# Kernel tuning notes

Hardware: AMD Instinct MI355X
Metric: run time of the kernel (lower is better)

Reference implementation:

```python
import jax, jax.numpy as jnp
import numpy as np

C = 128; L = 2; LMAX = 3; NB = 8
R_MAX = 5.0; P_CUT = 5.0; AVG_NEI = 16.0
DELTA_K = 0.2; K_CUT = 0.6; NKRBF = 128; DP = 8
B_GRAPHS = 8; N_ATOMS = 3200; N_EDGES = 51200; NEL = 10
SKIP = (2.0 + 1.0) ** -0.5  # skip_connection_factor with use_ewald=True
_LOFLM_NP = np.repeat(np.arange(4), [1, 3, 5, 7])  # l index of each of 16 lm slots
LOFLM = jnp.asarray(_LOFLM_NP)
LM1H = jnp.asarray(np.eye(4, dtype=np.float32)[_LOFLM_NP])  # [16,4] one-hot lm->l


def _k_grid_np():
    r = np.arange(-3, 4)
    g = np.stack(np.meshgrid(r, r, r, indexing='ij'), -1).reshape(-1, 3).astype(np.float32) * DELTA_K
    return g[np.linalg.norm(g, axis=1) <= K_CUT + 1e-6]  # [K,3], K=123


def _k_rbf_np(kg):
    d = np.linalg.norm(kg, axis=1)
    c = np.linspace(0.0, K_CUT, NKRBF).astype(np.float32)
    w = c[1] - c[0]
    return np.exp(-0.5 * ((d[:, None] - c[None, :]) / w) ** 2).astype(np.float32)


def _sph_harm(u):
    # real spherical harmonics, e3nn 'component' normalization, l=0..3 -> 16 comps
    x, y, z = u[:, 0], u[:, 1], u[:, 2]
    s3, s5, s15 = 3.0 ** 0.5, 5.0 ** 0.5, 15.0 ** 0.5
    c70, c105, c42, c7 = 70.0 ** 0.5 / 4.0, 105.0 ** 0.5, 42.0 ** 0.5 / 4.0, 7.0 ** 0.5 / 2.0
    comps = [jnp.ones_like(x),
             s3 * x, s3 * y, s3 * z,
             s15 * x * y, s15 * y * z, 0.5 * s5 * (3 * z * z - 1.0), s15 * x * z, 0.5 * s15 * (x * x - y * y),
             c70 * y * (3 * x * x - y * y), c105 * x * y * z, c42 * y * (5 * z * z - 1.0),
             c7 * z * (5 * z * z - 3.0), c42 * x * (5 * z * z - 1.0), 0.5 * c105 * z * (x * x - y * y),
             c70 * x * (x * x - 3 * y * y)]
    return jnp.stack(comps, axis=-1)


def _radial(r):
    # Bessel basis * polynomial cutoff envelope (p=5)
    n = jnp.arange(1, NB + 1, dtype=r.dtype)
    rb = jnp.sqrt(2.0 / R_MAX) * jnp.sin(n * jnp.pi * r[:, None] / R_MAX) / jnp.maximum(r, 1e-9)[:, None]
    uu = jnp.clip(r / R_MAX, 0.0, 1.0)
    p = P_CUT
    env = 1.0 - (p + 1.0) * (p + 2.0) / 2.0 * uu ** 5 + p * (p + 2.0) * uu ** 6 - p * (p + 1.0) / 2.0 * uu ** 7
    env = env * (r < R_MAX)
    return rb * env[:, None]


def _forward(positions, node_attrs, shifts, edge_index, batch, kgrid, krbf, W_embed, atomic_E, rW1, rb1, rW2, rb2, rW3, rb3, rW4, Wup, w2, w3, Wmix, Wr0, Wr1a, Wr1b, Wdown, WupE, Wpre1, bpre1, Wpre2, bpre2, Wm1, bm1, Wm2, bm2):
    silu = jax.nn.silu
    src, dst = edge_index[0], edge_index[1]
    vec = positions[dst] - positions[src] + shifts            # [E,3]
    r = jnp.linalg.norm(vec, axis=1)
    uvec = vec / jnp.maximum(r, 1e-9)[:, None]
    Y = _sph_harm(uvec)                                       # [E,16]
    ef = _radial(r)                                           # [E,8]
    h = node_attrs @ W_embed                                  # [N,C]
    e0 = jax.ops.segment_sum(node_attrs @ atomic_E, batch, num_segments=B_GRAPHS)
    # Ewald precompute (shared across layers, as in the torch code: dot/sinc computed once)
    dot = positions @ kgrid.T                                 # [N,K]
    sd = jnp.prod(jnp.sinc(0.5 * DELTA_K * positions), axis=1, keepdims=True)  # [N,1]
    cosd = sd * jnp.cos(dot)
    sind = sd * jnp.sin(dot)
    kdown = krbf @ Wdown                                      # [K,DP]
    energy = e0
    for i in range(L):
        # ---- Ewald block ----
        hres = h + silu(h @ Wpre1[i] + bpre1[i]) @ Wpre2[i] + bpre2[i]
        kfilter = kdown @ WupE[i]                             # [K,C]
        sfr = jax.ops.segment_sum(hres[:, None, :] * cosd[:, :, None], batch, num_segments=B_GRAPHS)  # [B,K,C]
        sfi = jax.ops.segment_sum(hres[:, None, :] * sind[:, :, None], batch, num_segments=B_GRAPHS)
        he = 0.01 * (jnp.einsum('nk,nkc->nc', cosd, (sfr * kfilter)[batch])
                     + jnp.einsum('nk,nkc->nc', sind, (sfi * kfilter)[batch]))
        he = silu(he @ Wm1[i] + bm1[i])
        he = silu(he @ Wm2[i] + bm2[i])
        # ---- equivariant interaction (channelwise TP with SH, radial-MLP weights) ----
        hu = h @ Wup[i]
        w = silu(ef @ rW1[i] + rb1[i])
        w = silu(w @ rW2[i] + rb2[i])
        w = silu(w @ rW3[i] + rb3[i])
        w = (w @ rW4[i]).reshape(-1, C, LMAX + 1)             # [E,C,4] per-(channel,l) weights
        we = jnp.take(w, LOFLM, axis=2)                       # [E,C,16]
        msg = we * hu[src][:, :, None] * Y[:, None, :]        # [E,C,16]
        A = jax.ops.segment_sum(msg, dst, num_segments=positions.shape[0]) / AVG_NEI  # [N,C,16]
        # ---- product basis (invariant contractions up to correlation 3) + residual sc ----
        scal = A[:, :, 0]
        inv2 = jnp.einsum('ncs,sl->ncl', A * A, LM1H)         # [N,C,4] per-l norms
        feats = scal + jnp.einsum('ncl,lc->nc', inv2, w2[i]) + scal * jnp.einsum('ncl,lc->nc', inv2, w3[i])
        hprod = feats @ Wmix[i] + h
        h = SKIP * (hprod + he)
        # ---- readout ----
        if i < L - 1:
            node_e = (h @ Wr0)[:, 0]
        else:
            node_e = (silu(h @ Wr1a) @ Wr1b)[:, 0]
        energy = energy + jax.ops.segment_sum(node_e, batch, num_segments=B_GRAPHS)
    return energy  # [B]


def setup_inputs() -> dict:
    ks = jax.random.split(jax.random.key(0), 32)
    def rn(i, shape, scale):
        return jax.random.normal(ks[i], shape, jnp.float32) * scale
    d = {}
    d['positions'] = jax.random.normal(ks[0], (N_ATOMS, 3), jnp.float32)
    d['node_attrs'] = jax.random.uniform(ks[1], (N_ATOMS, NEL), dtype=jnp.float32)
    d['shifts'] = jnp.zeros((N_EDGES, 3), jnp.float32)
    d['edge_index'] = jax.random.randint(ks[2], (2, N_EDGES), 0, N_ATOMS)
    d['batch'] = jnp.sort(jax.random.randint(ks[3], (N_ATOMS,), 0, B_GRAPHS))
    kg = _k_grid_np()
    d['kgrid'] = jnp.asarray(kg)
    d['krbf'] = jnp.asarray(_k_rbf_np(kg))
    d['W_embed'] = rn(4, (NEL, C), NEL ** -0.5)
    d['atomic_E'] = rn(5, (NEL,), 1.0)
    d['rW1'] = rn(6, (L, NB, 64), NB ** -0.5)
    d['rb1'] = jnp.zeros((L, 64), jnp.float32)
    d['rW2'] = rn(7, (L, 64, 64), 64 ** -0.5)
    d['rb2'] = jnp.zeros((L, 64), jnp.float32)
    d['rW3'] = rn(8, (L, 64, 64), 64 ** -0.5)
    d['rb3'] = jnp.zeros((L, 64), jnp.float32)
    d['rW4'] = rn(9, (L, 64, C * (LMAX + 1)), 64 ** -0.5)
    d['Wup'] = rn(10, (L, C, C), C ** -0.5)
    d['w2'] = rn(11, (L, LMAX + 1, C), 0.1)
    d['w3'] = rn(12, (L, LMAX + 1, C), 0.1)
    d['Wmix'] = rn(13, (L, C, C), C ** -0.5)
    d['Wr0'] = rn(14, (C, 1), C ** -0.5)
    d['Wr1a'] = rn(15, (C, 16), C ** -0.5)
    d['Wr1b'] = rn(16, (16, 1), 16 ** -0.5)
    d['Wdown'] = rn(17, (NKRBF, DP), NKRBF ** -0.5)
    d['WupE'] = rn(18, (L, DP, C), DP ** -0.5)
    d['Wpre1'] = rn(19, (L, C, C), C ** -0.5)
    d['bpre1'] = jnp.zeros((L, C), jnp.float32)
    d['Wpre2'] = rn(20, (L, C, C), C ** -0.5)
    d['bpre2'] = jnp.zeros((L, C), jnp.float32)
    d['Wm1'] = rn(21, (L, C, C), C ** -0.5)
    d['bm1'] = jnp.zeros((L, C), jnp.float32)
    d['Wm2'] = rn(22, (L, C, C), C ** -0.5)
    d['bm2'] = jnp.zeros((L, C), jnp.float32)
    return d


def reference(positions, node_attrs, shifts, edge_index, batch, kgrid, krbf, W_embed, atomic_E, rW1, rb1, rW2, rb2, rW3, rb3, rW4, Wup, w2, w3, Wmix, Wr0, Wr1a, Wr1b, Wdown, WupE, Wpre1, bpre1, Wpre2, bpre2, Wm1, bm1, Wm2, bm2):
    return _forward(positions, node_attrs, shifts, edge_index, batch, kgrid, krbf, W_embed, atomic_E, rW1, rb1, rW2, rb2, rW3, rb3, rW4, Wup, w2, w3, Wmix, Wr0, Wr1a, Wr1b, Wdown, WupE, Wpre1, bpre1, Wpre2, bpre2, Wm1, bm1, Wm2, bm2)
```

## Files before the change

kernel.cpp:

```cpp
#include <hip/hip_runtime.h>
#include <hip/hip_bf16.h>
#include <math.h>

constexpr int NA  = 3200;
constexpr int NE  = 51200;
constexpr int C   = 128;
constexpr int NK  = 123;
constexpr int NKP = 128;
constexpr int BG  = 8;
constexpr int SFSPLIT = 8;
constexpr float SKIPF = 0.57735026918962576f;
constexpr float AVGN  = 16.0f;
constexpr size_t SFSZ = (size_t)BG * NK * C;

__device__ __forceinline__ float dsilu(float x) { return x / (1.0f + expf(-x)); }

__device__ __forceinline__ unsigned short f2bf(float f) {
    unsigned int u = __float_as_uint(f);
    unsigned int r = (u + 0x7fffu + ((u >> 16) & 1u)) >> 16;
    return (unsigned short)r;
}
__device__ __forceinline__ float bf2f(unsigned short s) {
    return __uint_as_float(((unsigned int)s) << 16);
}

typedef __attribute__((ext_vector_type(8))) short short8;
typedef __attribute__((ext_vector_type(4))) float f32x4;

template <int K, int ACT, int OBF16, int LB = 0>
__global__ __launch_bounds__(256, 4) void gemm_kernel(
    const float* __restrict__ X, const float* __restrict__ W,
    const float* __restrict__ bias, void* __restrict__ outv,
    int M, int N)
{
    if (LB) {
        int L = blockIdx.z;
        W += (size_t)L * K * N;
        if (bias) bias += (size_t)L * N;
        outv = OBF16 ? (void*)((unsigned short*)outv + (size_t)L * M * N)
                     : (void*)((float*)outv + (size_t)L * M * N);
    }
    constexpr int K4 = K / 4;
    constexpr int BK  = (K < 64) ? K : 64;
    constexpr int BK4 = BK / 4;
    constexpr int BK4P = BK4 + 1;
    __shared__ float As[64 * BK4P * 4];
    __shared__ float Bs[BK * 64];
    const int tid = threadIdx.x;
    const int m0 = blockIdx.x * 64;
    const int n0 = blockIdx.y * 64;

    const float4* X4 = (const float4*)X;
    const float4* W4 = (const float4*)W;
    float4* As4 = (float4*)As;
    float4* Bs4 = (float4*)Bs;
    const int N4 = N >> 2;

    const int tx = tid & 15;
    const int ty = tid >> 4;
    float acc[4][4];
#pragma unroll
    for (int i = 0; i < 4; i++)
#pragma unroll
        for (int j = 0; j < 4; j++) acc[i][j] = 0.0f;

    for (int k0 = 0; k0 < K4; k0 += BK4) {
        if (k0) __syncthreads();
        for (int idx = tid; idx < 64 * BK4; idx += 256) {
            int r = idx / BK4, k4 = idx - r * BK4;
            As4[r * BK4P + k4] = X4[(size_t)(m0 + r) * K4 + k0 + k4];
        }
        for (int idx = tid; idx < BK * 16; idx += 256) {
            int kr = idx >> 4, c4 = idx & 15;
            Bs4[idx] = W4[(size_t)(k0 * 4 + kr) * N4 + (n0 >> 2) + c4];
        }
        __syncthreads();

#pragma unroll 4
        for (int k4 = 0; k4 < BK4; k4++) {
            float a[4][4];
#pragma unroll
            for (int i = 0; i < 4; i++) {
                float4 av = As4[(ty * 4 + i) * BK4P + k4];
                a[i][0] = av.x; a[i][1] = av.y; a[i][2] = av.z; a[i][3] = av.w;
            }
#pragma unroll
            for (int kk = 0; kk < 4; kk++) {
                float4 bv = Bs4[(k4 * 4 + kk) * 16 + tx];
#pragma unroll
                for (int i = 0; i < 4; i++) {
                    acc[i][0] += a[i][kk] * bv.x;
                    acc[i][1] += a[i][kk] * bv.y;
                    acc[i][2] += a[i][kk] * bv.z;
                    acc[i][3] += a[i][kk] * bv.w;
                }
            }
        }
    }

    float4 bv = make_float4(0.f, 0.f, 0.f, 0.f);
    if (bias) bv = ((const float4*)bias)[(n0 >> 2) + tx];
#pragma unroll
    for (int i = 0; i < 4; i++) {
        int row = m0 + ty * 4 + i;
        size_t o = (size_t)row * N + n0 + tx * 4;
        float4 v;
        v.x = acc[i][0] + bv.x; v.y = acc[i][1] + bv.y;
        v.z = acc[i][2] + bv.z; v.w = acc[i][3] + bv.w;
        if (ACT) { v.x = dsilu(v.x); v.y = dsilu(v.y); v.z = dsilu(v.z); v.w = dsilu(v.w); }
        if (OBF16) {
            ushort4 pk;
            pk.x = f2bf(v.x); pk.y = f2bf(v.y); pk.z = f2bf(v.z); pk.w = f2bf(v.w);
            *(ushort4*)((unsigned short*)outv + o) = pk;
        } else {
            *(float4*)((float*)outv + o) = v;
        }
    }
}

__global__ __launch_bounds__(256, 2) void k_pre(
    const float* __restrict__ h,
    const unsigned short* __restrict__ W1t, const float* __restrict__ b1,
    const unsigned short* __restrict__ Wut,
    const unsigned short* __restrict__ W2t, const float* __restrict__ b2,
    float* __restrict__ hu, float* __restrict__ hres)
{
    constexpr int MT = 32, ASH = 136;
    __shared__ unsigned short Xs[MT * ASH];
    __shared__ unsigned short Ts[MT * ASH];
    __shared__ unsigned short Ws[128 * ASH];
    const int tid = threadIdx.x;
    const int m0 = blockIdx.x * MT;

    for (int idx = tid; idx < MT * 32; idx += 256) {
        int r = idx >> 5, c4 = idx & 31;
        float4 v = ((const float4*)h)[(size_t)(m0 + r) * 32 + c4];
        ushort4 pk;
        pk.x = f2bf(v.x); pk.y = f2bf(v.y); pk.z = f2bf(v.z); pk.w = f2bf(v.w);
        *(ushort4*)(Xs + r * ASH + c4 * 4) = pk;
    }
    for (int idx = tid; idx < 128 * 16; idx += 256) {
        int r = idx >> 4, s = idx & 15;
        *(short8*)(Ws + r * ASH + s * 8) = ((const short8*)W1t)[(size_t)r * 16 + s];
    }
    __syncthreads();

    const int wave = tid >> 6;
    const int lane = tid & 63;
    const int q = lane >> 4;
    const int l16 = lane & 15;
    const int mh = (wave & 1) * 16;
    const int nh = (wave >> 1) * 64;

    f32x4 acc[4];
#pragma unroll
    for (int ni = 0; ni < 4; ni++) acc[ni] = (f32x4){0.f, 0.f, 0.f, 0.f};
#pragma unroll
    for (int kc = 0; kc < 4; kc++) {
        short8 a = *(const short8*)(Xs + (mh + l16) * ASH + kc * 32 + q * 8);
#pragma unroll
        for (int ni = 0; ni < 4; ni++) {
            short8 b = *(const short8*)(Ws + (nh + ni * 16 + l16) * ASH + kc * 32 + q * 8);
            acc[ni] = __builtin_amdgcn_mfma_f32_16x16x32_bf16(a, b, acc[ni], 0, 0, 0);
        }
    }
#pragma unroll
    for (int ni = 0; ni < 4; ni++) {
        float bv = b1[nh + ni * 16 + l16];
#pragma unroll
        for (int r = 0; r < 4; r++)
            Ts[(mh + q * 4 + r) * ASH + nh + ni * 16 + l16] = f2bf(dsilu(acc[ni][r] + bv));
    }
    __syncthreads();
    for (int idx = tid; idx < 128 * 16; idx += 256) {
        int r = idx >> 4, s = idx & 15;
        *(short8*)(Ws + r * ASH + s * 8) = ((const short8*)Wut)[(size_t)r * 16 + s];
    }
    __syncthreads();
#pragma unroll
    for (int ni = 0; ni < 4; ni++) acc[ni] = (f32x4){0.f, 0.f, 0.f, 0.f};
#pragma unroll
    for (int kc = 0; kc < 4; kc++) {
        short8 a = *(const short8*)(Xs + (mh + l16) * ASH + kc * 32 + q * 8);
#pragma unroll
        for (int ni = 0; ni < 4; ni++) {
            short8 b = *(const short8*)(Ws + (nh + ni * 16 + l16) * ASH + kc * 32 + q * 8);
            acc[ni] = __builtin_amdgcn_mfma_f32_16x16x32_bf16(a, b, acc[ni], 0, 0, 0);
        }
    }
#pragma unroll
    for (int ni = 0; ni < 4; ni++) {
#pragma unroll
        for (int r = 0; r < 4; r++)
            hu[(size_t)(m0 + mh + q * 4 + r) * C + nh + ni * 16 + l16] = acc[ni][r];
    }
    __syncthreads();
    for (int idx = tid; idx < 128 * 16; idx += 256) {
        int r = idx >> 4, s = idx & 15;
        *(short8*)(Ws + r * ASH + s * 8) = ((const short8*)W2t)[(size_t)r * 16 + s];
    }
    __syncthreads();
#pragma unroll
    for (int ni = 0; ni < 4; ni++) acc[ni] = (f32x4){0.f, 0.f, 0.f, 0.f};
#pragma unroll
    for (int kc = 0; kc < 4; kc++) {
        short8 a = *(const short8*)(Ts + (mh + l16) * ASH + kc * 32 + q * 8);
#pragma unroll
        for (int ni = 0; ni < 4; ni++) {
            short8 b = *(const short8*)(Ws + (nh + ni * 16 + l16) * ASH + kc * 32 + q * 8);
            acc[ni] = __builtin_amdgcn_mfma_f32_16x16x32_bf16(a, b, acc[ni], 0, 0, 0);
        }
    }
#pragma unroll
    for (int ni = 0; ni < 4; ni++) {
        float bv = b2[nh + ni * 16 + l16];
#pragma unroll
        for (int r = 0; r < 4; r++) {
            int row = m0 + mh + q * 4 + r;
            int col = nh + ni * 16 + l16;
            hres[(size_t)row * C + col] = acc[ni][r] + bv + h[(size_t)row * C + col];
        }
    }
}

__global__ __launch_bounds__(128, 2) void k_mlp_mfma(
    const unsigned short* __restrict__ X, const unsigned short* __restrict__ Wbase,
    const float* __restrict__ bbase, unsigned short* __restrict__ out)
{
    constexpr int MT = 128, AS = 72;
    __shared__ unsigned short Als[MT * AS];
    __shared__ unsigned short Bls[64 * AS];
    const int tid = threadIdx.x;
    const int m0 = blockIdx.x * MT;
    const int layer = (m0 >= NE) ? 1 : 0;
    const unsigned short* Wt = Wbase + (size_t)layer * 64 * 64;
    const float* bias = bbase + (size_t)layer * 64;

    for (int idx = tid; idx < MT * 8; idx += 128) {
        int r = idx >> 3, s = idx & 7;
        *(short8*)(Als + r * AS + s * 8) = ((const short8*)X)[(size_t)(m0 + r) * 8 + s];
    }
    for (int idx = tid; idx < 64 * 8; idx += 128) {
        int r = idx >> 3, s = idx & 7;
        *(short8*)(Bls + r * AS + s * 8) = ((const short8*)Wt)[(size_t)r * 8 + s];
    }
    __syncthreads();

    const int wave = tid >> 6;
    const int lane = tid & 63;
    const int q = lane >> 4;
    const int l16 = lane & 15;
    const int mw = wave * 64;

    f32x4 acc[4][4];
#pragma unroll
    for (int mi = 0; mi < 4; mi++)
#pragma unroll
        for (int ni = 0; ni < 4; ni++) acc[mi][ni] = (f32x4){0.f, 0.f, 0.f, 0.f};

#pragma unroll
    for (int kc = 0; kc < 2; kc++) {
        short8 a[4], b[4];
#pragma unroll
        for (int mi = 0; mi < 4; mi++)
            a[mi] = *(const short8*)(Als + (mw + mi * 16 + l16) * AS + kc * 32 + q * 8);
#pragma unroll
        for (int ni = 0; ni < 4; ni++)
            b[ni] = *(const short8*)(Bls + (ni * 16 + l16) * AS + kc * 32 + q * 8);
#pragma unroll
        for (int mi = 0; mi < 4; mi++)
#pragma unroll
            for (int ni = 0; ni < 4; ni++)
                acc[mi][ni] = __builtin_amdgcn_mfma_f32_16x16x32_bf16(a[mi], b[ni], acc[mi][ni], 0, 0, 0);
    }

#pragma unroll
    for (int ni = 0; ni < 4; ni++) {
        float bv = bias[ni * 16 + l16];
#pragma unroll
        for (int mi = 0; mi < 4; mi++) {
#pragma unroll
            for (int r = 0; r < 4; r++) {
                int e = m0 + mw + mi * 16 + q * 4 + r;
                int n = ni * 16 + l16;
                out[(size_t)e * 64 + n] = f2bf(dsilu(acc[mi][ni][r] + bv));
            }
        }
    }
}

__global__ __launch_bounds__(256, 2) void k_wbuf_mfma(
    const unsigned short* __restrict__ X, const unsigned short* __restrict__ W4base,
    unsigned short* __restrict__ wbuf)
{
    constexpr int MT = 256, NT = 64, AS = 72;
    __shared__ unsigned short Als[MT * AS];
    __shared__ unsigned short Bls[NT * AS];
    const int tid = threadIdx.x;
    const int m0 = blockIdx.x * MT;
    const int n0 = blockIdx.y * NT;
    const int layer = (m0 >= NE) ? 1 : 0;
    const unsigned short* W4t = W4base + (size_t)layer * 512 * 64;

    for (int idx = tid; idx < MT * 8; idx += 256) {
        int r = idx >> 3, s = idx & 7;
        *(short8*)(Als + r * AS + s * 8) = ((const short8*)X)[(size_t)(m0 + r) * 8 + s];
    }
    for (int idx = tid; idx < NT * 8; idx += 256) {
        int r = idx >> 3, s = idx & 7;
        *(short8*)(Bls + r * AS + s * 8) = ((const short8*)W4t)[(size_t)(n0 + r) * 8 + s];
    }
    __syncthreads();

    const int wave = tid >> 6;
    const int lane = tid & 63;
    const int q = lane >> 4;
    const int l16 = lane & 15;
    const int mw = wave * 64;

    f32x4 acc[4][4];
#pragma unroll
    for (int mi = 0; mi < 4; mi++)
#pragma unroll
        for (int ni = 0; ni < 4; ni++) acc[mi][ni] = (f32x4){0.f, 0.f, 0.f, 0.f};

#pragma unroll
    for (int kc = 0; kc < 2; kc++) {
        short8 a[4], b[4];
#pragma unroll
        for (int mi = 0; mi < 4; mi++)
            a[mi] = *(const short8*)(Als + (mw + mi * 16 + l16) * AS + kc * 32 + q * 8);
#pragma unroll
        for (int ni = 0; ni < 4; ni++)
            b[ni] = *(const short8*)(Bls + (ni * 16 + l16) * AS + kc * 32 + q * 8);
#pragma unroll
        for (int mi = 0; mi < 4; mi++)
#pragma unroll
            for (int ni = 0; ni < 4; ni++)
                acc[mi][ni] = __builtin_amdgcn_mfma_f32_16x16x32_bf16(a[mi], b[ni], acc[mi][ni], 0, 0, 0);
    }

#pragma unroll
    for (int mi = 0; mi < 4; mi++) {
#pragma unroll
        for (int ni = 0; ni < 4; ni++) {
#pragma unroll
            for (int r = 0; r < 4; r++) {
                int e = m0 + mw + mi * 16 + q * 4 + r;
                int n = n0 + ni * 16 + l16;
                wbuf[(size_t)e * 512 + n] = f2bf(acc[mi][ni][r]);
            }
        }
    }
}

constexpr int TK0 = NA;
constexpr int TK1 = TK0 + 8;
constexpr int TK2 = TK1 + 512;
constexpr int TK3 = TK2 + 64;
constexpr int TK4 = TK3 + 64;
constexpr int TK5 = TK4 + 256;
constexpr int TK6 = TK5 + 256;
constexpr int TK7 = TK6 + 256;
constexpr int TK8 = TK7 + 256;
constexpr int TK9 = TK8 + 256;
constexpr int TKEND = TK9 + 1;

__device__ __forceinline__ float sincn(float x) {
    float px = 3.14159265358979323846f * x;
    return (fabsf(px) < 1e-8f) ? 1.0f : (sinf(px) / px);
}

__device__ __forceinline__ void convT128_task(
    const float* __restrict__ W, unsigned short* __restrict__ Wt, int idx)
{
    int layer = idx >> 14, rem = idx & 16383;
    int n = rem >> 7, k = rem & 127;
    Wt[((size_t)layer << 14) + (n << 7) + k] = f2bf(W[((size_t)layer << 14) + (k << 7) + n]);
}

__global__ __launch_bounds__(128) void k_setup(
    const float* __restrict__ na, const float* __restrict__ Wemb,
    const float* __restrict__ aE, const int* __restrict__ batch,
    const float* __restrict__ pos, const float* __restrict__ kgrid,
    const float* __restrict__ krbf, const float* __restrict__ Wdown,
    const float* __restrict__ rW4, const float* __restrict__ rW2,
    const float* __restrict__ rW3, const float* __restrict__ Wm1,
    const float* __restrict__ Wm2, const float* __restrict__ Wpre1,
    const float* __restrict__ Wpre2, const float* __restrict__ Wup,
    float* __restrict__ h, float* __restrict__ e0buf,
    float* __restrict__ cosd, float* __restrict__ sind,
    unsigned short* __restrict__ cosdb, unsigned short* __restrict__ sindb,
    float* __restrict__ kdwn,
    unsigned short* __restrict__ W4bt, unsigned short* __restrict__ W2bt,
    unsigned short* __restrict__ W3bt, unsigned short* __restrict__ Wm1bt,
    unsigned short* __restrict__ Wm2bt, unsigned short* __restrict__ Wpre1bt,
    unsigned short* __restrict__ Wpre2bt, unsigned short* __restrict__ Wupbt,
    int* __restrict__ gs)
{
    const int bx = blockIdx.x;
    const int t = threadIdx.x;
    __shared__ int cnt[BG];

    if (bx < TK0) {
        int n = bx, c = t;
        float s = 0.f;
#pragma unroll
        for (int k = 0; k < 10; k++) s += na[n * 10 + k] * Wemb[k * C + c];
        h[(size_t)n * C + c] = s;
        if (c == 0) {
            float e = 0.f;
#pragma unroll
            for (int k = 0; k < 10; k++) e += na[n * 10 + k] * aE[k];
            e0buf[n] = e;
        }
        float p0 = pos[n * 3 + 0], p1 = pos[n * 3 + 1], p2 = pos[n * 3 + 2];
        float sd = sincn(0.1f * p0) * sincn(0.1f * p1) * sincn(0.1f * p2);
        int k = t;
        float cv = 0.f, sv = 0.f;
        if (k < NK) {
            float d = p0 * kgrid[k * 3 + 0] + p1 * kgrid[k * 3 + 1] + p2 * kgrid[k * 3 + 2];
            float sn, cs;
            sincosf(d, &sn, &cs);
            cv = sd * cs;
            sv = sd * sn;
        }
        cosd[(size_t)n * NKP + k] = cv;
        sind[(size_t)n * NKP + k] = sv;
        cosdb[(size_t)n * NKP + k] = f2bf(cv);
        sindb[(size_t)n * NKP + k] = f2bf(sv);
    } else if (bx < TK1) {
        int slot = (bx - TK0) * 128 + t;
        if (slot < NK * 8) {
            int k = slot >> 3, j = slot & 7;
            float s = 0.f;
            for (int r = 0; r < 128; r++) s += krbf[k * 128 + r] * Wdown[r * 8 + j];
            kdwn[slot] = s;
        }
    } else if (bx < TK2) {
        int idx = (bx - TK1) * 128 + t;
        int layer = idx >> 15, rem = idx & 32767;
        int n = rem >> 6, k = rem & 63;
        W4bt[((size_t)layer * 512 + n) * 64 + k] = f2bf(rW4[((size_t)layer * 64 + k) * 512 + n]);
    } else if (bx < TK3) {
        int idx = (bx - TK2) * 128 + t;
        int layer = idx >> 12, rem = idx & 4095;
        int n = rem >> 6, k = rem & 63;
        W2bt[((size_t)layer * 64 + n) * 64 + k] = f2bf(rW2[((size_t)layer * 64 + k) * 64 + n]);
    } else if (bx < TK4) {
        int idx = (bx - TK3) * 128 + t;
        int layer = idx >> 12, rem = idx & 4095;
        int n = rem >> 6, k = rem & 63;
        W3bt[((size_t)layer * 64 + n) * 64 + k] = f2bf(rW3[((size_t)layer * 64 + k) * 64 + n]);
    } else if (bx < TK5) {
        convT128_task(Wm1, Wm1bt, (bx - TK4) * 128 + t);
    } else if (bx < TK6) {
        convT128_task(Wm2, Wm2bt, (bx - TK5) * 128 + t);
    } else if (bx < TK7) {
        convT128_task(Wpre1, Wpre1bt, (bx - TK6) * 128 + t);
    } else if (bx < TK8) {
        convT128_task(Wpre2, Wpre2bt, (bx - TK7) * 128 + t);
    } else if (bx < TK9) {
        convT128_task(Wup, Wupbt, (bx - TK8) * 128 + t);
    } else {
        if (t < BG) cnt[t] = 0;
        __syncthreads();
        for (int n = t; n < NA; n += 128) atomicAdd(&cnt[batch[n]], 1);
        __syncthreads();
        if (t == 0) {
            int s = 0;
            for (int b = 0; b < BG; b++) { gs[b] = s; s += cnt[b]; }
            gs[BG] = s;
        }
    }
}

__global__ __launch_bounds__(256) void k_edge_geom(
    const float* __restrict__ pos, const float* __restrict__ shifts,
    const int* __restrict__ eidx, float* __restrict__ Y, float* __restrict__ ef,
    int* __restrict__ deg)
{
    int e = blockIdx.x * 256 + threadIdx.x;
    if (e >= NE) return;
    int s = eidx[e], d = eidx[NE + e];
    atomicAdd(&deg[d], 1);
    float vx = pos[d * 3 + 0] - pos[s * 3 + 0] + shifts[e * 3 + 0];
    float vy = pos[d * 3 + 1] - pos[s * 3 + 1] + shifts[e * 3 + 1];
    float vz = pos[d * 3 + 2] - pos[s * 3 + 2] + shifts[e * 3 + 2];
    float r = sqrtf(vx * vx + vy * vy + vz * vz);
    float rinv = 1.0f / fmaxf(r, 1e-9f);
    float x = vx * rinv, y = vy * rinv, z = vz * rinv;

    const float s3 = 1.7320508075688772f, s5 = 2.2360679774997896f, s15 = 3.8729833462074170f;
    const float c70 = 2.0916500663351889f;
    const float c105 = 10.246950765959598f;
    const float c42 = 1.6201851746019651f;
    const float c7 = 1.3228756555322954f;
    float o[16];
    o[0] = 1.0f;
    o[1] = s3 * x; o[2] = s3 * y; o[3] = s3 * z;
    o[4] = s15 * x * y; o[5] = s15 * y * z; o[6] = 0.5f * s5 * (3.f * z * z - 1.f);
    o[7] = s15 * x * z; o[8] = 0.5f * s15 * (x * x - y * y);
    o[9]  = c70 * y * (3.f * x * x - y * y);
    o[10] = c105 * x * y * z;
    o[11] = c42 * y * (5.f * z * z - 1.f);
    o[12] = c7 * z * (5.f * z * z - 3.f);
    o[13] = c42 * x * (5.f * z * z - 1.f);
    o[14] = 0.5f * c105 * z * (x * x - y * y);
    o[15] = c70 * x * (x * x - 3.f * y * y);
    float4* Y4 = (float4*)(Y + (size_t)e * 16);
    Y4[0] = make_float4(o[0], o[1], o[2], o[3]);
    Y4[1] = make_float4(o[4], o[5], o[6], o[7]);
    Y4[2] = make_float4(o[8], o[9], o[10], o[11]);
    Y4[3] = make_float4(o[12], o[13], o[14], o[15]);

    float uu = fminf(fmaxf(r * 0.2f, 0.f), 1.f);
    float u2 = uu * uu, u4 = u2 * u2, u5 = u4 * uu, u6 = u5 * uu, u7 = u6 * uu;
    float env = 1.f - 21.f * u5 + 35.f * u6 - 15.f * u7;
    env = (r < 5.0f) ? env : 0.0f;
    float pref = 0.63245553203367587f * rinv * env;
    const float pio5 = 0.62831853071795865f;
    float efv[8];
#pragma unroll
    for (int n1 = 1; n1 <= 8; n1++) efv[n1 - 1] = pref * sinf(n1 * pio5 * r);
    float4* E4 = (float4*)(ef + (size_t)e * 8);
    E4[0] = make_float4(efv[0], efv[1], efv[2], efv[3]);
    E4[1] = make_float4(efv[4], efv[5], efv[6], efv[7]);
}

__global__ __launch_bounds__(1024) void k_scan(
    const int* __restrict__ deg, int* __restrict__ offs, int* __restrict__ cursor)
{
    __shared__ int sc[1024];
    int tid = threadIdx.x;
    int base = tid * 4;
    int v[4]; int s = 0;
#pragma unroll
    for (int i = 0; i < 4; i++) {
        int idx = base + i;
        int d = (idx < NA) ? deg[idx] : 0;
        v[i] = s; s += d;
    }
    sc[tid] = s;
    __syncthreads();
    for (int ofs = 1; ofs < 1024; ofs <<= 1) {
        int t = (tid >= ofs) ? sc[tid - ofs] : 0;
        __syncthreads();
        sc[tid] += t;
        __syncthreads();
    }
    int excl = (tid > 0) ? sc[tid - 1] : 0;
#pragma unroll
    for (int i = 0; i < 4; i++) {
        int idx = base + i;
        if (idx < NA) { int o = excl + v[i]; offs[idx] = o; cursor[idx] = o; }
    }
    if (tid == 1023) offs[NA] = sc[1023];
}

__global__ __launch_bounds__(256) void k_fill(
    const int* __restrict__ eidx, int* __restrict__ cursor, int* __restrict__ perm)
{
    int e = blockIdx.x * 256 + threadIdx.x;
    if (e < NE) {
        int d = eidx[NE + e];
        int p = atomicAdd(&cursor[d], 1);
        perm[p] = e;
    }
}

__global__ __launch_bounds__(256, 4) void k_sf(
    const float* __restrict__ hres, const float* __restrict__ cosd, const float* __restrict__ sind,
    const int* __restrict__ gs, const float* __restrict__ kdwn, const float* __restrict__ WupE,
    float* __restrict__ sfp)
{
    const int b = blockIdx.x, kt = blockIdx.y, sp = blockIdx.z;
    const int n0 = gs[b], n1 = gs[b + 1];
    const int cnt = n1 - n0;
    const int per = (cnt + SFSPLIT - 1) / SFSPLIT;
    const int cs = n0 + sp * per;
    const int ce = min(cs + per, n1);

    __shared__ float Hs[32 * 128];
    __shared__ float Cs[32 * 32];
    __shared__ float Ss[32 * 32];

    const int tid = threadIdx.x;
    const int tx = tid & 31;
    const int ty = tid >> 5;

    float accR[4][4], accI[4][4];
#pragma unroll
    for (int i = 0; i < 4; i++)
#pragma unroll
        for (int j = 0; j < 4; j++) { accR[i][j] = 0.f; accI[i][j] = 0.f; }

    float4* H4 = (float4*)Hs;
    float4* C4 = (float4*)Cs;
    float4* S4 = (float4*)Ss;

    for (int nb = cs; nb < ce; nb += 32) {
        __syncthreads();
        for (int idx = tid; idx < 32 * 32; idx += 256) {
            int r = idx >> 5, c4 = idx & 31;
            int n = nb + r;
            H4[idx] = (n < ce) ? ((const float4*)hres)[(size_t)n * 32 + c4]
                               : make_float4(0.f, 0.f, 0.f, 0.f);
        }
        for (int idx = tid; idx < 32 * 8; idx += 256) {
            int r = idx >> 3, k4 = idx & 7;
            int n = nb + r;
            float4 cv = make_float4(0.f, 0.f, 0.f, 0.f), sv = cv;
            if (n < ce) {
                cv = ((const float4*)cosd)[(size_t)n * 32 + kt * 8 + k4];
                sv = ((const float4*)sind)[(size_t)n * 32 + kt * 8 + k4];
            }
            C4[idx] = cv;
            S4[idx] = sv;
        }
        __syncthreads();
        const int lim = min(32, ce - nb);
        for (int n = 0; n < lim; n++) {
            float4 hv = H4[n * 32 + tx];
            float4 cv = C4[n * 8 + ty];
            float4 sv = S4[n * 8 + ty];
            float h[4] = { hv.x, hv.y, hv.z, hv.w };
            float ck[4] = { cv.x, cv.y, cv.z, cv.w };
            float sk[4] = { sv.x, sv.y, sv.z, sv.w };
#pragma unroll
            for (int i = 0; i < 4; i++)
#pragma unroll
                for (int j = 0; j < 4; j++) {
                    accR[i][j] += ck[i] * h[j];
                    accI[i][j] += sk[i] * h[j];
                }
        }
    }

    const int kbase = kt * 32 + ty * 4;
    float* baseR = sfp + (size_t)sp * SFSZ;
    float* baseI = sfp + (size_t)(SFSPLIT + sp) * SFSZ;
#pragma unroll
    for (int i = 0; i < 4; i++) {
        int k = kbase + i;
        if (k < NK) {
            float4 kfv = make_float4(0.f, 0.f, 0.f, 0.f);
#pragma unroll
            for (int j = 0; j < 8; j++) {
                float kd = kdwn[k * 8 + j];
                float4 wv = ((const float4*)WupE)[(size_t)j * 32 + tx];
                kfv.x += kd * wv.x; kfv.y += kd * wv.y;
                kfv.z += kd * wv.z; kfv.w += kd * wv.w;
            }
            float vx = kfv.x * 0.01f, vy = kfv.y * 0.01f, vz = kfv.z * 0.01f, vw = kfv.w * 0.01f;
            size_t o = ((size_t)(b * NK + k)) * C + tx * 4;
            *(float4*)(baseR + o) = make_float4(accR[i][0] * vx, accR[i][1] * vy,
                                                accR[i][2] * vz, accR[i][3] * vw);
            *(float4*)(baseI + o) = make_float4(accI[i][0] * vx, accI[i][1] * vy,
                                                accI[i][2] * vz, accI[i][3] * vw);
        }
    }
}

__global__ __launch_bounds__(256) void k_sfredT(
    const float* __restrict__ sfp,
    unsigned short* __restrict__ sfrT, unsigned short* __restrict__ sfiT)
{
    const int kc = blockIdx.x * 16;
    const int b = blockIdx.y;
    __shared__ float Tr[16 * 128];
    __shared__ float Ti[16 * 128];
    const int tid = threadIdx.x;
    const size_t S4 = SFSZ / 4;
    const float4* P4 = (const float4*)sfp;

    for (int idx = tid; idx < 16 * 32; idx += 256) {
        int kk = idx >> 5, c4 = idx & 31;
        float4 ar = make_float4(0.f, 0.f, 0.f, 0.f), ai = ar;
        if (kc + kk < NK) {
            size_t off = ((size_t)(b * NK + kc + kk)) * 32 + c4;
#pragma unroll
            for (int sp = 0; sp < SFSPLIT; sp++) {
                float4 r = P4[(size_t)sp * S4 + off];
                ar.x += r.x; ar.y += r.y; ar.z += r.z; ar.w += r.w;
                float4 q = P4[(size_t)(SFSPLIT + sp) * S4 + off];
                ai.x += q.x; ai.y += q.y; ai.z += q.z; ai.w += q.w;
            }
        }
        ((float4*)Tr)[idx] = ar;
        ((float4*)Ti)[idx] = ai;
    }
    __syncthreads();
    const int c = tid & 127;
    const int sel = tid >> 7;
    const float* T = sel ? Ti : Tr;
    unsigned short* out = sel ? sfiT : sfrT;
    unsigned short tmp[16];
#pragma unroll
    for (int kk = 0; kk < 16; kk++) tmp[kk] = f2bf(T[kk * 128 + c]);
    short8* dst = (short8*)(out + ((size_t)(b * 128 + c)) * NKP + kc);
    dst[0] = *(short8*)(tmp);
    dst[1] = *(short8*)(tmp + 8);
}

__global__ __launch_bounds__(256) void k_he_mlp(
    const unsigned short* __restrict__ cosdb, const unsigned short* __restrict__ sindb,
    const unsigned short* __restrict__ sfrT, const unsigned short* __restrict__ sfiT,
    const int* __restrict__ gs,
    const unsigned short* __restrict__ Wm1t, const float* __restrict__ bm1,
    const unsigned short* __restrict__ Wm2t, const float* __restrict__ bm2,
    float* __restrict__ he2)
{
    constexpr int ASH = 136;
    constexpr int BSH = 72;
    __shared__ __align__(16) char smem[54272];
    unsigned short* Ca = (unsigned short*)smem;
    unsigned short* Sa = (unsigned short*)(smem + 8704);
    unsigned short* Br = (unsigned short*)(smem + 17408);
    unsigned short* Bi = (unsigned short*)(smem + 35840);
    unsigned short* Xs = (unsigned short*)smem;
    unsigned short* Ts = (unsigned short*)(smem + 8704);
    unsigned short* Ws = (unsigned short*)(smem + 17408);

    const int b = blockIdx.y;
    const int a0g = gs[b], a1g = gs[b + 1];
    const int a0 = a0g + blockIdx.x * 32;
    if (a0 >= a1g) return;
    const int nal = min(32, a1g - a0);
    const int tid = threadIdx.x;

    const short8 z8 = (short8){0,0,0,0,0,0,0,0};
    for (int idx = tid; idx < 32 * 16; idx += 256) {
        int r = idx >> 4, s = idx & 15;
        short8 cv = z8, sv = z8;
        if (r < nal) {
            cv = ((const short8*)cosdb)[(size_t)(a0 + r) * 16 + s];
            sv = ((const short8*)sindb)[(size_t)(a0 + r) * 16 + s];
        }
        *(short8*)(Ca + r * ASH + s * 8) = cv;
        *(short8*)(Sa + r * ASH + s * 8) = sv;
    }

    const int wave = tid >> 6;
    const int lane = tid & 63;
    const int q = lane >> 4;
    const int l16 = lane & 15;
    const int mh = (wave & 1) * 16;
    const int nh = (wave >> 1) * 64;

    f32x4 acc[4];
#pragma unroll
    for (int ni = 0; ni < 4; ni++) acc[ni] = (f32x4){0.f, 0.f, 0.f, 0.f};

#pragma unroll
    for (int kc2 = 0; kc2 < 2; kc2++) {
        __syncthreads();
        for (int idx = tid; idx < 128 * 8; idx += 256) {
            int c = idx >> 3, s = idx & 7;
            size_t gi = (size_t)(b * 128 + c) * 16 + kc2 * 8 + s;
            *(short8*)(Br + c * BSH + s * 8) = ((const short8*)sfrT)[gi];
            *(short8*)(Bi + c * BSH + s * 8) = ((const short8*)sfiT)[gi];
        }
        __syncthreads();
#pragma unroll
        for (int ks = 0; ks < 2; ks++) {
            short8 ar = *(const short8*)(Ca + (mh + l16) * ASH + kc2 * 64 + ks * 32 + q * 8);
            short8 ai = *(const short8*)(Sa + (mh + l16) * ASH + kc2 * 64 + ks * 32 + q * 8);
#pragma unroll
            for (int ni = 0; ni < 4; ni++) {
                short8 br = *(const short8*)(Br + (nh + ni * 16 + l16) * BSH + ks * 32 + q * 8);
                acc[ni] = __builtin_amdgcn_mfma_f32_16x16x32_bf16(ar, br, acc[ni], 0, 0, 0);
                short8 bi = *(const short8*)(Bi + (nh + ni * 16 + l16) * BSH + ks * 32 + q * 8);
                acc[ni] = __builtin_amdgcn_mfma_f32_16x16x32_bf16(ai, bi, acc[ni], 0, 0, 0);
            }
        }
    }
    __syncthreads();

#pragma unroll
    for (int ni = 0; ni < 4; ni++) {
#pragma unroll
        for (int r = 0; r < 4; r++)
            Xs[(mh + q * 4 + r) * ASH + nh + ni * 16 + l16] = f2bf(acc[ni][r]);
    }
    __syncthreads();
    for (int idx = tid; idx < 128 * 16; idx += 256) {
        int r = idx >> 4, s = idx & 15;
        *(short8*)(Ws + r * ASH + s * 8) = ((const short8*)Wm1t)[(size_t)r * 16 + s];
    }
    __syncthreads();

    f32x4 acc2[4];
#pragma unroll
    for (int ni = 0; ni < 4; ni++) acc2[ni] = (f32x4){0.f, 0.f, 0.f, 0.f};
#pragma unroll
    for (int kc = 0; kc < 4; kc++) {
        short8 a = *(const short8*)(Xs + (mh + l16) * ASH + kc * 32 + q * 8);
#pragma unroll
        for (int ni = 0; ni < 4; ni++) {
            short8 bb = *(const short8*)(Ws + (nh + ni * 16 + l16) * ASH + kc * 32 + q * 8);
            acc2[ni] = __builtin_amdgcn_mfma_f32_16x16x32_bf16(a, bb, acc2[ni], 0, 0, 0);
        }
    }
#pragma unroll
    for (int ni = 0; ni < 4; ni++) {
        float bv = bm1[nh + ni * 16 + l16];
#pragma unroll
        for (int r = 0; r < 4; r++)
            Ts[(mh + q * 4 + r) * ASH + nh + ni * 16 + l16] = f2bf(dsilu(acc2[ni][r] + bv));
    }
    __syncthreads();
    for (int idx = tid; idx < 128 * 16; idx += 256) {
        int r = idx >> 4, s = idx & 15;
        *(short8*)(Ws + r * ASH + s * 8) = ((const short8*)Wm2t)[(size_t)r * 16 + s];
    }
    __syncthreads();
#pragma unroll
    for (int ni = 0; ni < 4; ni++) acc2[ni] = (f32x4){0.f, 0.f, 0.f, 0.f};
#pragma unroll
    for (int kc = 0; kc < 4; kc++) {
        short8 a = *(const short8*)(Ts + (mh + l16) * ASH + kc * 32 + q * 8);
#pragma unroll
        for (int ni = 0; ni < 4; ni++) {
            short8 bb = *(const short8*)(Ws + (nh + ni * 16 + l16) * ASH + kc * 32 + q * 8);
            acc2[ni] = __builtin_amdgcn_mfma_f32_16x16x32_bf16(a, bb, acc2[ni], 0, 0, 0);
        }
    }
#pragma unroll
    for (int ni = 0; ni < 4; ni++) {
        int col = nh + ni * 16 + l16;
        float bv = bm2[col];
#pragma unroll
        for (int r = 0; r < 4; r++) {
            int lrow = mh + q * 4 + r;
            if (lrow < nal)
                he2[(size_t)(a0 + lrow) * C + col] = dsilu(acc2[ni][r] + bv);
        }
    }
}

__global__ __launch_bounds__(128) void k_gather_mix(
    const unsigned short* __restrict__ wbuf, const float* __restrict__ hu,
    const float* __restrict__ Y, const int* __restrict__ srcArr,
    const int* __restrict__ offs, const int* __restrict__ perm,
    const float* __restrict__ w2, const float* __restrict__ w3,
    const float* __restrict__ Wmix, const float* __restrict__ h,
    const float* __restrict__ he2,
    const float* __restrict__ Wr0, const float* __restrict__ Wr1a,
    const float* __restrict__ Wr1b, int mode,
    float* __restrict__ hn, float* __restrict__ nebuf)
{
    int n = blockIdx.x, c = threadIdx.x;
    int j0 = offs[n], j1 = offs[n + 1];
    float A[16];
#pragma unroll
    for (int s = 0; s < 16; s++) A[s] = 0.f;
    for (int j = j0; j < j1; j++) {
        int e = perm[j];
        int s = srcArr[e];
        float huc = hu[(size_t)s * C + c];
        ushort4 wv = *(const ushort4*)(wbuf + (size_t)e * 512 + c * 4);
        const float4* Yp = (const float4*)(Y + (size_t)e * 16);
        float4 y0 = Yp[0], y1 = Yp[1], y2 = Yp[2], y3 = Yp[3];
        float m0 = bf2f(wv.x) * huc, m1 = bf2f(wv.y) * huc;
        float m2 = bf2f(wv.z) * huc, m3 = bf2f(wv.w) * huc;
        A[0] += m0 * y0.x;
        A[1] += m1 * y0.y;  A[2]  += m1 * y0.z;  A[3]  += m1 * y0.w;
        A[4] += m2 * y1.x;  A[5]  += m2 * y1.y;  A[6]  += m2 * y1.z;  A[7] += m2 * y1.w;
        A[8] += m2 * y2.x;
        A[9] += m3 * y2.y;  A[10] += m3 * y2.z;  A[11] += m3 * y2.w;
        A[12] += m3 * y3.x; A[13] += m3 * y3.y;  A[14] += m3 * y3.z;  A[15] += m3 * y3.w;
    }
    const float inv = 1.0f / AVGN;
#pragma unroll
    for (int s = 0; s < 16; s++) A[s] *= inv;
    float scal = A[0];
    float i0 = A[0] * A[0];
    float i1 = A[1] * A[1] + A[2] * A[2] + A[3] * A[3];
    float i2 = A[4] * A[4] + A[5] * A[5] + A[6] * A[6] + A[7] * A[7] + A[8] * A[8];
    float i3 = A[9] * A[9] + A[10] * A[10] + A[11] * A[11] + A[12] * A[12] +
               A[13] * A[13] + A[14] * A[14] + A[15] * A[15];
    float t2 = i0 * w2[c] + i1 * w2[C + c] + i2 * w2[2 * C + c] + i3 * w2[3 * C + c];
    float t3 = i0 * w3[c] + i1 * w3[C + c] + i2 * w3[2 * C + c] + i3 * w3[3 * C + c];
    float fe_c = scal + t2 + scal * t3;

    __shared__ float fs[128];
    __shared__ float red[16];
    fs[c] = fe_c;
    __syncthreads();

    float mix = 0.f;
#pragma unroll 8
    for (int k = 0; k < 128; k++) mix += fs[k] * Wmix[(size_t)k * C + c];

    float hnv = SKIPF * (mix + h[(size_t)n * C + c] + he2[(size_t)n * C + c]);
    hn[(size_t)n * C + c] = hnv;

    __syncthreads();
    fs[c] = hnv;
    __syncthreads();

    if (mode == 0) {
        float v = hnv * Wr0[c];
#pragma unroll
        for (int o = 32; o; o >>= 1) v += __shfl_down(v, o, 64);
        if ((c & 63) == 0) red[c >> 6] = v;
        __syncthreads();
        if (c == 0) nebuf[n] = red[0] + red[1];
    } else {
        if (c < 16) {
            float s = 0.f;
#pragma unroll 8
            for (int cc = 0; cc < 128; cc++) s += fs[cc] * Wr1a[cc * 16 + c];
            red[c] = dsilu(s) * Wr1b[c];
        }
        __syncthreads();
        if (c == 0) {
            float s = 0.f;
#pragma unroll
            for (int j = 0; j < 16; j++) s += red[j];
            nebuf[n] = s;
        }
    }
}

__global__ __launch_bounds__(256) void k_reduceE(
    const float* __restrict__ e0buf, const float* __restrict__ nebuf,
    const int* __restrict__ gs, float* __restrict__ Eout)
{
    int b = blockIdx.x, t = threadIdx.x;
    int n0 = gs[b], n1 = gs[b + 1];
    float s = 0.f;
    for (int n = n0 + t; n < n1; n += 256)
        s += e0buf[n] + nebuf[n] + nebuf[NA + n];
#pragma unroll
    for (int o = 32; o; o >>= 1) s += __shfl_down(s, o, 64);
    __shared__ float red[4];
    if ((t & 63) == 0) red[t >> 6] = s;
    __syncthreads();
    if (t == 0) Eout[b] = red[0] + red[1] + red[2] + red[3];
}

constexpr size_t NAC   = (size_t)NA * C;
constexpr size_t F_COSD = 0;
constexpr size_t F_SIND = F_COSD + (size_t)NA * NKP;
constexpr size_t F_Y    = F_SIND + (size_t)NA * NKP;
constexpr size_t F_EF   = F_Y + (size_t)NE * 16;
constexpr size_t F_H    = F_EF + (size_t)NE * 8;
constexpr size_t F_HN   = F_H + NAC;
constexpr size_t F_HRES = F_HN + NAC;
constexpr size_t F_T1   = F_HRES + NAC;
constexpr size_t F_HE2  = F_T1 + NAC;
constexpr size_t F_HU   = F_HE2 + NAC;
constexpr size_t F_TA   = F_HU + NAC;
constexpr size_t F_TB   = F_TA + (size_t)NE * 64;
constexpr size_t F_WTS  = F_TB + (size_t)NE * 64;
constexpr size_t F_W    = F_WTS + 128 * 1024;
constexpr size_t F_SFR  = F_W + (size_t)NE * 512;
constexpr size_t F_SFI  = F_SFR + SFSZ;
constexpr size_t F_SFP  = F_SFI + SFSZ;
constexpr size_t F_KD   = F_SFP + 2 * (size_t)SFSPLIT * SFSZ;
constexpr size_t F_E0   = F_KD + 1024;
constexpr size_t F_NE   = F_E0 + NA;
constexpr size_t F_CB   = F_NE + 2 * (size_t)NA;
constexpr size_t F_SB   = F_CB + (size_t)NA * 64;
constexpr size_t F_END  = F_SB + (size_t)NA * 64;
constexpr size_t I_BASE = ((F_END * 4 + 255) / 256) * 256;

extern "C" void kernel_launch(void* const* d_in, const int* in_sizes, int n_in,
                              void* d_out, int out_size, void* d_ws, size_t ws_size,
                              hipStream_t stream) {
    const float* pos    = (const float*)d_in[0];
    const float* na     = (const float*)d_in[1];
    const float* shifts = (const float*)d_in[2];
    const int*   eidx   = (const int*)d_in[3];
    const int*   batch  = (const int*)d_in[4];
    const float* kgrid  = (const float*)d_in[5];
    const float* krbf   = (const float*)d_in[6];
    const float* Wemb   = (const float*)d_in[7];
    const float* aE     = (const float*)d_in[8];
    const float* rW1    = (const float*)d_in[9];
    const float* rb1    = (const float*)d_in[10];
    const float* rW2    = (const float*)d_in[11];
    const float* rb2    = (const float*)d_in[12];
    const float* rW3    = (const float*)d_in[13];
    const float* rb3    = (const float*)d_in[14];
    const float* rW4    = (const float*)d_in[15];
    const float* Wup    = (const float*)d_in[16];
    const float* w2     = (const float*)d_in[17];
    const float* w3     = (const float*)d_in[18];
    const float* Wmix   = (const float*)d_in[19];
    const float* Wr0    = (const float*)d_in[20];
    const float* Wr1a   = (const float*)d_in[21];
    const float* Wr1b   = (const float*)d_in[22];
    const float* Wdown  = (const float*)d_in[23];
    const float* WupE   = (const float*)d_in[24];
    const float* Wpre1  = (const float*)d_in[25];
    const float* bpre1  = (const float*)d_in[26];
    const float* Wpre2  = (const float*)d_in[27];
    const float* bpre2  = (const float*)d_in[28];
    const float* Wm1    = (const float*)d_in[29];
    const float* bm1    = (const float*)d_in[30];
    const float* Wm2    = (const float*)d_in[31];
    const float* bm2    = (const float*)d_in[32];

    float* fw = (float*)d_ws;
    float* cosd = fw + F_COSD;
    float* sind = fw + F_SIND;
    float* Ybuf = fw + F_Y;
    float* efb  = fw + F_EF;
    float* h    = fw + F_H;
    float* hn   = fw + F_HN;
    float* hres = fw + F_HRES;
    float* he2  = fw + F_HE2;
    float* hu   = fw + F_HU;
    unsigned short* tA   = (unsigned short*)(fw + F_TA);
    unsigned short* hbuf = (unsigned short*)(fw + F_TB);
    unsigned short* W4bt = (unsigned short*)(fw + F_WTS);
    unsigned short* W2bt  = W4bt + (size_t)2 * 512 * 64;
    unsigned short* W3bt  = W2bt + (size_t)2 * 64 * 64;
    unsigned short* Wm1bt = W3bt + (size_t)2 * 64 * 64;
    unsigned short* Wm2bt = Wm1bt + (size_t)2 * 128 * 128;
    unsigned short* Wp1bt = Wm2bt + (size_t)2 * 128 * 128;
    unsigned short* Wp2bt = Wp1bt + (size_t)2 * 128 * 128;
    unsigned short* Wupbt = Wp2bt + (size_t)2 * 128 * 128;
    unsigned short* wbuf = (unsigned short*)(fw + F_W);
    unsigned short* sfrT = (unsigned short*)(fw + F_SFR);
    unsigned short* sfiT = (unsigned short*)(fw + F_SFI);
    float* sfp  = fw + F_SFP;
    float* kdwn = fw + F_KD;
    float* e0buf = fw + F_E0;
    float* nebuf = fw + F_NE;
    unsigned short* cosdb = (unsigned short*)(fw + F_CB);
    unsigned short* sindb = (unsigned short*)(fw + F_SB);

    int* ip     = (int*)((char*)d_ws + I_BASE);
    int* deg    = ip;
    int* offs   = ip + NA;
    int* cursor = ip + 2 * NA + 1;
    int* perm   = ip + 3 * NA + 1;
    int* gs     = perm + NE;

    float* Eout = (float*)d_out;

    hipMemsetAsync(deg, 0, NA * sizeof(int), stream);

    k_setup<<<TKEND, 128, 0, stream>>>(
        na, Wemb, aE, batch, pos, kgrid, krbf, Wdown,
        rW4, rW2, rW3, Wm1, Wm2, Wpre1, Wpre2, Wup,
        h, e0buf, cosd, sind, cosdb, sindb, kdwn,
        W4bt, W2bt, W3bt, Wm1bt, Wm2bt, Wp1bt, Wp2bt, Wupbt, gs);
    k_edge_geom<<<NE / 256, 256, 0, stream>>>(pos, shifts, eidx, Ybuf, efb, deg);
    k_scan<<<1, 1024, 0, stream>>>(deg, offs, cursor);
    k_fill<<<NE / 256, 256, 0, stream>>>(eidx, cursor, perm);

    gemm_kernel<8, 1, 1, 1><<<dim3(NE / 64, 1, 2), 256, 0, stream>>>(
        efb, rW1, rb1, hbuf, NE, 64);
    k_mlp_mfma<<<2 * NE / 128, 128, 0, stream>>>(hbuf, W2bt, rb2, tA);
    k_mlp_mfma<<<2 * NE / 128, 128, 0, stream>>>(tA, W3bt, rb3, hbuf);
    k_wbuf_mfma<<<dim3(2 * NE / 256, 512 / 64), 256, 0, stream>>>(hbuf, W4bt, wbuf);

    const dim3 gSF(BG, 4, SFSPLIT);
    const dim3 gRT(8, BG);
    const dim3 gHE(16, BG);

    for (int i = 0; i < 2; i++) {
        const float* bpre1_i = bpre1 + (size_t)i * C;
        const float* bpre2_i = bpre2 + (size_t)i * C;
        const float* WupE_i  = WupE + (size_t)i * 8 * C;
        const float* bm1_i   = bm1 + (size_t)i * C;
        const float* bm2_i   = bm2 + (size_t)i * C;
        const float* w2_i    = w2 + (size_t)i * 4 * C;
        const float* w3_i    = w3 + (size_t)i * 4 * C;
        const float* Wmix_i  = Wmix + (size_t)i * C * C;
        const unsigned short* Wm1bt_i = Wm1bt + (size_t)i * 128 * 128;
        const unsigned short* Wm2bt_i = Wm2bt + (size_t)i * 128 * 128;
        const unsigned short* Wp1bt_i = Wp1bt + (size_t)i * 128 * 128;
        const unsigned short* Wp2bt_i = Wp2bt + (size_t)i * 128 * 128;
        const unsigned short* Wupbt_i = Wupbt + (size_t)i * 128 * 128;
        const unsigned short* wbuf_i = wbuf + (size_t)i * NE * 512;

        k_pre<<<NA / 32, 256, 0, stream>>>(h, Wp1bt_i, bpre1_i, Wupbt_i,
                                           Wp2bt_i, bpre2_i, hu, hres);

        k_sf<<<gSF, 256, 0, stream>>>(hres, cosd, sind, gs, kdwn, WupE_i, sfp);
        k_sfredT<<<gRT, 256, 0, stream>>>(sfp, sfrT, sfiT);
        k_he_mlp<<<gHE, 256, 0, stream>>>(cosdb, sindb, sfrT, sfiT, gs,
                                          Wm1bt_i, bm1_i, Wm2bt_i, bm2_i, he2);

        k_gather_mix<<<NA, 128, 0, stream>>>(wbuf_i, hu, Ybuf, eidx, offs, perm,
                                             w2_i, w3_i, Wmix_i, h, he2,
                                             Wr0, Wr1a, Wr1b, (i == 0) ? 0 : 1,
                                             hn, nebuf + (size_t)i * NA);

        float* tmp = h; h = hn; hn = tmp;
    }

    k_reduceE<<<BG, 256, 0, stream>>>(e0buf, nebuf, gs, Eout);
}
```

Before: 345.2 us.

## Store per-edge data in destination-sorted order to make gathers contiguous

Edge geometry is now computed after the CSR sort, and the spherical harmonics, radial features, and everything derived from them (the MLP weights in wbuf) are written in destination-sorted order. The gather kernel then reads wbuf and Y contiguously by CSR position, and reads sources from a precomputed sorted srcP array instead of going through perm indirection. This removes scattered accesses to large per-edge buffers in the gather, at the cost of an extra count kernel and a serialized edge-geometry launch.

```diff
diff --git a/kernel.cpp b/kernel.cpp
--- a/kernel.cpp
+++ b/kernel.cpp
@@ -475,15 +475,64 @@
     }
 }
 
+__global__ __launch_bounds__(256) void k_count(const int* __restrict__ eidx, int* __restrict__ deg)
+{
+    int e = blockIdx.x * 256 + threadIdx.x;
+    if (e < NE) atomicAdd(&deg[eidx[NE + e]], 1);
+}
+
+__global__ __launch_bounds__(1024) void k_scan(
+    const int* __restrict__ deg, int* __restrict__ offs, int* __restrict__ cursor)
+{
+    __shared__ int sc[1024];
+    int tid = threadIdx.x;
+    int base = tid * 4;
+    int v[4]; int s = 0;
+#pragma unroll
+    for (int i = 0; i < 4; i++) {
+        int idx = base + i;
+        int d = (idx < NA) ? deg[idx] : 0;
+        v[i] = s; s += d;
+    }
+    sc[tid] = s;
+    __syncthreads();
+    for (int ofs = 1; ofs < 1024; ofs <<= 1) {
+        int t = (tid >= ofs) ? sc[tid - ofs] : 0;
+        __syncthreads();
+        sc[tid] += t;
+        __syncthreads();
+    }
+    int excl = (tid > 0) ? sc[tid - 1] : 0;
+#pragma unroll
+    for (int i = 0; i < 4; i++) {
+        int idx = base + i;
+        if (idx < NA) { int o = excl + v[i]; offs[idx] = o; cursor[idx] = o; }
+    }
+    if (tid == 1023) offs[NA] = sc[1023];
+}
+
+__global__ __launch_bounds__(256) void k_fill(
+    const int* __restrict__ eidx, int* __restrict__ cursor,
+    int* __restrict__ perm, int* __restrict__ srcP)
+{
+    int e = blockIdx.x * 256 + threadIdx.x;
+    if (e < NE) {
+        int d = eidx[NE + e];
+        int p = atomicAdd(&cursor[d], 1);
+        perm[p] = e;
+        srcP[p] = eidx[e];
+    }
+}
+
 __global__ __launch_bounds__(256) void k_edge_geom(
     const float* __restrict__ pos, const float* __restrict__ shifts,
-    const int* __restrict__ eidx, float* __restrict__ Y, float* __restrict__ ef,
-    int* __restrict__ deg)
-{
-    int e = blockIdx.x * 256 + threadIdx.x;
-    if (e >= NE) return;
+    const int* __restrict__ eidx, const int* __restrict__ perm,
+    float* __restrict__ Y, float* __restrict__ ef)
+{
+    int j = blockIdx.x * 256 + threadIdx.x;
+    if (j >= NE) return;
+    int e = perm[j];
     int s = eidx[e], d = eidx[NE + e];
-    atomicAdd(&deg[d], 1);
     float vx = pos[d * 3 + 0] - pos[s * 3 + 0] + shifts[e * 3 + 0];
     float vy = pos[d * 3 + 1] - pos[s * 3 + 1] + shifts[e * 3 + 1];
     float vz = pos[d * 3 + 2] - pos[s * 3 + 2] + shifts[e * 3 + 2];
@@ -508,7 +557,7 @@
     o[13] = c42 * x * (5.f * z * z - 1.f);
     o[14] = 0.5f * c105 * z * (x * x - y * y);
     o[15] = c70 * x * (x * x - 3.f * y * y);
-    float4* Y4 = (float4*)(Y + (size_t)e * 16);
+    float4* Y4 = (float4*)(Y + (size_t)j * 16);
     Y4[0] = make_float4(o[0], o[1], o[2], o[3]);
     Y4[1] = make_float4(o[4], o[5], o[6], o[7]);
     Y4[2] = make_float4(o[8], o[9], o[10], o[11]);
@@ -523,50 +572,9 @@
     float efv[8];
 #pragma unroll
     for (int n1 = 1; n1 <= 8; n1++) efv[n1 - 1] = pref * sinf(n1 * pio5 * r);
-    float4* E4 = (float4*)(ef + (size_t)e * 8);
+    float4* E4 = (float4*)(ef + (size_t)j * 8);
     E4[0] = make_float4(efv[0], efv[1], efv[2], efv[3]);
     E4[1] = make_float4(efv[4], efv[5], efv[6], efv[7]);
-}
-
-__global__ __launch_bounds__(1024) void k_scan(
-    const int* __restrict__ deg, int* __restrict__ offs, int* __restrict__ cursor)
-{
-    __shared__ int sc[1024];
-    int tid = threadIdx.x;
-    int base = tid * 4;
-    int v[4]; int s = 0;
-#pragma unroll
-    for (int i = 0; i < 4; i++) {
-        int idx = base + i;
-        int d = (idx < NA) ? deg[idx] : 0;
-        v[i] = s; s += d;
-    }
-    sc[tid] = s;
-    __syncthreads();
-    for (int ofs = 1; ofs < 1024; ofs <<= 1) {
-        int t = (tid >= ofs) ? sc[tid - ofs] : 0;
-        __syncthreads();
-        sc[tid] += t;
-        __syncthreads();
-    }
-    int excl = (tid > 0) ? sc[tid - 1] : 0;
-#pragma unroll
-    for (int i = 0; i < 4; i++) {
-        int idx = base + i;
-        if (idx < NA) { int o = excl + v[i]; offs[idx] = o; cursor[idx] = o; }
-    }
-    if (tid == 1023) offs[NA] = sc[1023];
-}
-
-__global__ __launch_bounds__(256) void k_fill(
-    const int* __restrict__ eidx, int* __restrict__ cursor, int* __restrict__ perm)
-{
-    int e = blockIdx.x * 256 + threadIdx.x;
-    if (e < NE) {
-        int d = eidx[NE + e];
-        int p = atomicAdd(&cursor[d], 1);
-        perm[p] = e;
-    }
 }
 
 __global__ __launch_bounds__(256, 4) void k_sf(
@@ -841,8 +849,8 @@
 
 __global__ __launch_bounds__(128) void k_gather_mix(
     const unsigned short* __restrict__ wbuf, const float* __restrict__ hu,
-    const float* __restrict__ Y, const int* __restrict__ srcArr,
-    const int* __restrict__ offs, const int* __restrict__ perm,
+    const float* __restrict__ Y, const int* __restrict__ srcP,
+    const int* __restrict__ offs,
     const float* __restrict__ w2, const float* __restrict__ w3,
     const float* __restrict__ Wmix, const float* __restrict__ h,
     const float* __restrict__ he2,
@@ -856,11 +864,10 @@
 #pragma unroll
     for (int s = 0; s < 16; s++) A[s] = 0.f;
     for (int j = j0; j < j1; j++) {
-        int e = perm[j];
-        int s = srcArr[e];
+        int s = srcP[j];
         float huc = hu[(size_t)s * C + c];
-        ushort4 wv = *(const ushort4*)(wbuf + (size_t)e * 512 + c * 4);
-        const float4* Yp = (const float4*)(Y + (size_t)e * 16);
+        ushort4 wv = *(const ushort4*)(wbuf + (size_t)j * 512 + c * 4);
+        const float4* Yp = (const float4*)(Y + (size_t)j * 16);
         float4 y0 = Yp[0], y1 = Yp[1], y2 = Yp[2], y3 = Yp[3];
         float m0 = bf2f(wv.x) * huc, m1 = bf2f(wv.y) * huc;
         float m2 = bf2f(wv.z) * huc, m3 = bf2f(wv.w) * huc;
@@ -1039,7 +1046,8 @@
     int* offs   = ip + NA;
     int* cursor = ip + 2 * NA + 1;
     int* perm   = ip + 3 * NA + 1;
-    int* gs     = perm + NE;
+    int* srcP   = perm + NE;
+    int* gs     = srcP + NE;
 
     float* Eout = (float*)d_out;
 
@@ -1050,9 +1058,10 @@
         rW4, rW2, rW3, Wm1, Wm2, Wpre1, Wpre2, Wup,
         h, e0buf, cosd, sind, cosdb, sindb, kdwn,
         W4bt, W2bt, W3bt, Wm1bt, Wm2bt, Wp1bt, Wp2bt, Wupbt, gs);
-    k_edge_geom<<<NE / 256, 256, 0, stream>>>(pos, shifts, eidx, Ybuf, efb, deg);
+    k_count<<<NE / 256, 256, 0, stream>>>(eidx, deg);
     k_scan<<<1, 1024, 0, stream>>>(deg, offs, cursor);
-    k_fill<<<NE / 256, 256, 0, stream>>>(eidx, cursor, perm);
+    k_fill<<<NE / 256, 256, 0, stream>>>(eidx, cursor, perm, srcP);
+    k_edge_geom<<<NE / 256, 256, 0, stream>>>(pos, shifts, eidx, perm, Ybuf, efb);
 
     gemm_kernel<8, 1, 1, 1><<<dim3(NE / 64, 1, 2), 256, 0, stream>>>(
         efb, rW1, rb1, hbuf, NE, 64);
@@ -1088,7 +1097,7 @@
         k_he_mlp<<<gHE, 256, 0, stream>>>(cosdb, sindb, sfrT, sfiT, gs,
                                           Wm1bt_i, bm1_i, Wm2bt_i, bm2_i, he2);
 
-        k_gather_mix<<<NA, 128, 0, stream>>>(wbuf_i, hu, Ybuf, eidx, offs, perm,
+        k_gather_mix<<<NA, 128, 0, stream>>>(wbuf_i, hu, Ybuf, srcP, offs,
                                              w2_i, w3_i, Wmix_i, h, he2,
                                              Wr0, Wr1a, Wr1b, (i == 0) ? 0 : 1,
                                              hn, nebuf + (size_t)i * NA);
```

After: 338.9 us. No clear change (-1.8%).
